# Kernel tuning notes

Hardware: AMD Instinct MI355X
Metric: run time of the kernel (lower is better)

Reference implementation:

```python
import jax, jax.numpy as jnp
import numpy as np

N = 50000    # num genes (nodes)
E = 500000   # edges per edge type
T = 2        # edge types
L = 2        # gnn layers
H = 4        # attention heads
D = 64       # per-head channels (hidden // heads)
HID = 256    # hidden channels
PRE_IN = 1024
OUT = 64
EPS = 1e-5
SLOPE = 0.2  # PyG GATv2 leaky_relu negative slope


def _layer_norm(x, g, b):
    mu = x.mean(-1, keepdims=True)
    v = x.var(-1, keepdims=True)
    return (x - mu) / jnp.sqrt(v + EPS) * g + b


def _seg_softmax(score, seg, n):
    m = jax.ops.segment_max(score, seg, num_segments=n)
    ex = jnp.exp(score - m[seg])
    den = jax.ops.segment_sum(ex, seg, num_segments=n)
    return ex / (den[seg] + 1e-16)


def _gatv2_projected(x, src, dst, Wl, Wr, att, bias, Wp, bp):
    # GATv2Conv (share_weights=False, concat heads) followed by Linear projection
    n = x.shape[0]
    xl = (x @ Wl).reshape(n, H, D)
    xr = (x @ Wr).reshape(n, H, D)
    hs = xl[src]                                   # [E,H,D] messages from source
    e = jax.nn.leaky_relu(hs + xr[dst], SLOPE)     # [E,H,D]
    score = jnp.einsum('ehd,hd->eh', e, att)       # [E,H]
    alpha = _seg_softmax(score, dst, n)            # softmax over in-edges of dst
    out = jax.ops.segment_sum(hs * alpha[:, :, None], dst, num_segments=n)
    out = out.reshape(n, H * D) + bias             # concat heads + conv bias
    return out @ Wp + bp                           # ProjectedGATConv linear


def setup_inputs() -> dict:
    key = jax.random.key(0)
    ks = jax.random.split(key, 20)
    s = 0.05
    return {
        'x': jax.random.normal(ks[0], (N, PRE_IN), dtype=jnp.float32),
        'edge_index_0': jax.random.randint(ks[1], (2, E), 0, N, dtype=jnp.int32),
        'edge_index_1': jax.random.randint(ks[2], (2, E), 0, N, dtype=jnp.int32),
        'pre_W0': jax.random.normal(ks[3], (PRE_IN, HID)) * s,
        'pre_b0': jnp.zeros((HID,)),
        'pre_g0': jnp.ones((HID,)),
        'pre_be0': jnp.zeros((HID,)),
        'pre_W1': jax.random.normal(ks[4], (HID, HID)) * s,
        'pre_b1': jnp.zeros((HID,)),
        'pre_g1': jnp.ones((HID,)),
        'pre_be1': jnp.zeros((HID,)),
        # HeteroGnn: L layers x T edge types of ProjectedGATConv(GATv2)
        'gat_Wl': jax.random.normal(ks[5], (L, T, HID, H * D)) * s,
        'gat_Wr': jax.random.normal(ks[6], (L, T, HID, H * D)) * s,
        'gat_att': jax.random.normal(ks[7], (L, T, H, D)) * 0.1,
        'gat_bias': jnp.zeros((L, T, H * D)),
        'proj_W': jax.random.normal(ks[8], (L, T, H * D, HID)) * s,
        'proj_b': jnp.zeros((L, T, HID)),
        # prediction head: Linear(HID,HID) + relu + Linear(HID,OUT)
        'head_W0': jax.random.normal(ks[9], (HID, HID)) * s,
        'head_b0': jnp.zeros((HID,)),
        'head_W1': jax.random.normal(ks[10], (HID, OUT)) * s,
        'head_b1': jnp.zeros((OUT,)),
    }


def reference(x, edge_index_0, edge_index_1, pre_W0, pre_b0, pre_g0, pre_be0,
              pre_W1, pre_b1, pre_g1, pre_be1, gat_Wl, gat_Wr, gat_att,
              gat_bias, proj_W, proj_b, head_W0, head_b0, head_W1, head_b1):
    loop = jnp.arange(N, dtype=edge_index_0.dtype)  # add_self_loops=True
    edges = [(jnp.concatenate([ei[0], loop]), jnp.concatenate([ei[1], loop]))
             for ei in (edge_index_0, edge_index_1)]
    # preprocessor MLP
    h = jax.nn.relu(_layer_norm(x @ pre_W0 + pre_b0, pre_g0, pre_be0))
    h = jax.nn.relu(_layer_norm(h @ pre_W1 + pre_b1, pre_g1, pre_be1))
    # hetero GAT stack, HeteroConv aggr='sum'
    for l in range(L):
        acc = jnp.zeros((N, HID), dtype=h.dtype)
        for t in range(T):
            src, dst = edges[t]
            acc = acc + _gatv2_projected(h, src, dst, gat_Wl[l, t], gat_Wr[l, t],
                                         gat_att[l, t], gat_bias[l, t],
                                         proj_W[l, t], proj_b[l, t])
        h = jax.nn.relu(acc)
    # prediction head
    h2 = jax.nn.relu(h @ head_W0 + head_b0)
    return h2 @ head_W1 + head_b1
```

## Files before the change

kernel.cpp:

```cpp
#include <hip/hip_runtime.h>
#include <hip/hip_bf16.h>
#include <math.h>

#define N_NODES 50000
#define MP      50048
#define E_EDGES 500000
#define EPRIME  (E_EDGES + N_NODES)
#define HID     256
#define PRE_IN  1024
#define OUT_DIM 64
#define NHEAD   4
#define DHEAD   64
#define LAYERS  2
#define NTYPES  2

#define SCAN_NBLK 49
#define NPAD      (SCAN_NBLK * 1024)

typedef __attribute__((ext_vector_type(8))) short short8v;
typedef __attribute__((ext_vector_type(4))) float f32x4;
typedef _Float16 h2v __attribute__((ext_vector_type(2)));
typedef _Float16 h8v __attribute__((ext_vector_type(8)));

__device__ __forceinline__ ushort f2bf(float f) {
  uint u = __float_as_uint(f);
  u += 0x7FFF + ((u >> 16) & 1);
  return (ushort)(u >> 16);
}
__device__ __forceinline__ float bf2f(ushort u) {
  return __uint_as_float(((uint)u) << 16);
}

template<bool AF32>
__global__ __launch_bounds__(256) void gemm_k(
    const void* __restrict__ Ap,
    const ushort* __restrict__ Bt,
    int K, int M, int N,
    float*  __restrict__ Cf,
    ushort* __restrict__ Cb,
    const float* __restrict__ bias,
    const float* __restrict__ bias2,
    int do_relu, int out_f16)
{
  __shared__ ushort As[128 * 32];
  __shared__ ushort Bs[64 * 32];
  const int tid = threadIdx.x;
  const int l   = tid & 63;
  const int w   = tid >> 6;
  const int wm  = w & 1;
  const int wn  = w >> 1;

  const int nwg  = gridDim.x * gridDim.y;
  const int orig = blockIdx.y * gridDim.x + blockIdx.x;
  const int qq   = nwg >> 3, rr = nwg & 7;
  const int xcd  = orig & 7;
  const int wgid = ((xcd < rr) ? xcd * (qq + 1) : rr * (qq + 1) + (xcd - rr) * qq)
                   + (orig >> 3);
  const int bm = (wgid / gridDim.x) * 128;
  const int bn = (wgid % gridDim.x) * 64;

  f32x4 acc[4][2];
#pragma unroll
  for (int m = 0; m < 4; m++)
#pragma unroll
    for (int n = 0; n < 2; n++) acc[m][n] = (f32x4){0.f, 0.f, 0.f, 0.f};

  const int srow  = l >> 2;
  const int sslot = l & 3;

  const int brow  = tid >> 2;
  const int bslot = tid & 3;
  const int bkc   = bslot ^ ((brow >> 1) & 3);

  float4 pf[2][2];
  if constexpr (AF32) {
#pragma unroll
    for (int i = 0; i < 2; i++) {
      const int row = w * 32 + i * 16 + srow;
      const int kc  = sslot ^ ((row >> 1) & 3);
      pf[i][0] = make_float4(0.f, 0.f, 0.f, 0.f);
      pf[i][1] = make_float4(0.f, 0.f, 0.f, 0.f);
      if (bm + row < M) {
        const float* ga = (const float*)Ap + (size_t)(bm + row) * K + kc * 8;
        pf[i][0] = *reinterpret_cast<const float4*>(ga);
        pf[i][1] = *reinterpret_cast<const float4*>(ga + 4);
      }
    }
  }

  for (int k0 = 0; k0 < K; k0 += 32) {
    {
      const ushort* gb = Bt + (size_t)(bn + brow) * K + k0 + bkc * 8;
      __builtin_amdgcn_global_load_lds(
          (const __attribute__((address_space(1))) uint*)gb,
          (__attribute__((address_space(3))) uint*)((char*)Bs + tid * 16), 16, 0, 0);
    }
    if constexpr (AF32) {
#pragma unroll
      for (int i = 0; i < 2; i++) {
        const int row = w * 32 + i * 16 + srow;
        const uint off = (uint)row * 64 + (uint)sslot * 16;
        short8v s;
        s[0] = (short)f2bf(pf[i][0].x); s[1] = (short)f2bf(pf[i][0].y);
        s[2] = (short)f2bf(pf[i][0].z); s[3] = (short)f2bf(pf[i][0].w);
        s[4] = (short)f2bf(pf[i][1].x); s[5] = (short)f2bf(pf[i][1].y);
        s[6] = (short)f2bf(pf[i][1].z); s[7] = (short)f2bf(pf[i][1].w);
        *reinterpret_cast<short8v*>((char*)As + off) = s;
      }
      if (k0 + 32 < K) {
#pragma unroll
        for (int i = 0; i < 2; i++) {
          const int row = w * 32 + i * 16 + srow;
          const int kc  = sslot ^ ((row >> 1) & 3);
          if (bm + row < M) {
            const float* ga = (const float*)Ap + (size_t)(bm + row) * K + (k0 + 32) + kc * 8;
            pf[i][0] = *reinterpret_cast<const float4*>(ga);
            pf[i][1] = *reinterpret_cast<const float4*>(ga + 4);
          }
        }
      }
    } else {
#pragma unroll
      for (int i = 0; i < 2; i++) {
        const int row = w * 32 + i * 16 + srow;
        const int kc  = sslot ^ ((row >> 1) & 3);
        const uint off = (uint)row * 64 + (uint)sslot * 16;
        const ushort* ga = (const ushort*)Ap + (size_t)(bm + row) * K + k0 + kc * 8;
        __builtin_amdgcn_global_load_lds(
            (const __attribute__((address_space(1))) uint*)ga,
            (__attribute__((address_space(3))) uint*)((char*)As + off), 16, 0, 0);
      }
    }
    __syncthreads();

    short8v a[4], b[2];
#pragma unroll
    for (int m = 0; m < 4; m++) {
      const int row = wm * 64 + m * 16 + (l & 15);
      const int kc  = (l >> 4) ^ ((row >> 1) & 3);
      a[m] = *(const short8v*)((const char*)As + row * 64 + kc * 16);
    }
#pragma unroll
    for (int n = 0; n < 2; n++) {
      const int row = wn * 32 + n * 16 + (l & 15);
      const int kc  = (l >> 4) ^ ((row >> 1) & 3);
      b[n] = *(const short8v*)((const char*)Bs + row * 64 + kc * 16);
    }
#pragma unroll
    for (int m = 0; m < 4; m++)
#pragma unroll
      for (int n = 0; n < 2; n++)
        acc[m][n] = __builtin_amdgcn_mfma_f32_16x16x32_bf16(a[m], b[n], acc[m][n], 0, 0, 0);
    __syncthreads();
  }

  const int crow0 = bm + wm * 64 + (l >> 4) * 4;
  const int ccol0 = bn + wn * 32 + (l & 15);
#pragma unroll
  for (int m = 0; m < 4; m++) {
#pragma unroll
    for (int j = 0; j < 4; j++) {
      const int grow = crow0 + m * 16 + j;
      if (grow < M) {
#pragma unroll
        for (int n = 0; n < 2; n++) {
          const int gcol = ccol0 + n * 16;
          if (gcol < N) {
            float v = acc[m][n][j];
            if (bias)  v += bias[gcol];
            if (bias2) v += bias2[gcol];
            if (do_relu) v = fmaxf(v, 0.f);
            if (Cf) Cf[(size_t)grow * N + gcol] = v;
            else if (out_f16) {
              _Float16 hv = (_Float16)v;
              Cb[(size_t)grow * N + gcol] = *(ushort*)&hv;
            } else {
              Cb[(size_t)grow * N + gcol] = f2bf(v);
            }
          }
        }
      }
    }
  }
}

__global__ void ln_relu(const float* __restrict__ in, ushort* __restrict__ out,
                        const float* __restrict__ g, const float* __restrict__ be, int n)
{
  int gid = blockIdx.x * blockDim.x + threadIdx.x;
  int row = gid >> 6;
  int lane = threadIdx.x & 63;
  if (row >= n) return;
  float4 v = *reinterpret_cast<const float4*>(in + (size_t)row * HID + lane * 4);
  float s = v.x + v.y + v.z + v.w;
  float ss = v.x * v.x + v.y * v.y + v.z * v.z + v.w * v.w;
#pragma unroll
  for (int o = 1; o < 64; o <<= 1) { s += __shfl_xor(s, o); ss += __shfl_xor(ss, o); }
  float mu = s * (1.f / 256.f);
  float var = ss * (1.f / 256.f) - mu * mu;
  float inv = rsqrtf(var + 1e-5f);
  float4 gg = *reinterpret_cast<const float4*>(g + lane * 4);
  float4 bb = *reinterpret_cast<const float4*>(be + lane * 4);
  ushort4 o4;
  o4.x = f2bf(fmaxf((v.x - mu) * inv * gg.x + bb.x, 0.f));
  o4.y = f2bf(fmaxf((v.y - mu) * inv * gg.y + bb.y, 0.f));
  o4.z = f2bf(fmaxf((v.z - mu) * inv * gg.z + bb.z, 0.f));
  o4.w = f2bf(fmaxf((v.w - mu) * inv * gg.w + bb.w, 0.f));
  *reinterpret_cast<ushort4*>(out + (size_t)row * HID + lane * 4) = o4;
}

__global__ void csr_count2(const int* __restrict__ ei0, const int* __restrict__ ei1,
                           int* __restrict__ cnt0, int* __restrict__ cnt1)
{
  int e = blockIdx.x * blockDim.x + threadIdx.x;
  if (e >= 2 * EPRIME) return;
  int type = e >= EPRIME;
  int i = type ? e - EPRIME : e;
  const int* ei = type ? ei1 : ei0;
  int* cnt = type ? cnt1 : cnt0;
  int d = (i < E_EDGES) ? ei[E_EDGES + i] : (i - E_EDGES);
  atomicAdd(&cnt[d], 1);
}

__global__ __launch_bounds__(256) void scan_p1(const int* __restrict__ cnt0,
                                               const int* __restrict__ cnt1,
                                               int* __restrict__ bsums)
{
  int type = blockIdx.x >= SCAN_NBLK;
  int blk = type ? blockIdx.x - SCAN_NBLK : blockIdx.x;
  const int* cnt = type ? cnt1 : cnt0;
  int4 v = reinterpret_cast<const int4*>(cnt)[blk * 256 + threadIdx.x];
  int s = v.x + v.y + v.z + v.w;
#pragma unroll
  for (int o = 1; o < 64; o <<= 1) s += __shfl_xor(s, o);
  __shared__ int wt[4];
  if ((threadIdx.x & 63) == 0) wt[threadIdx.x >> 6] = s;
  __syncthreads();
  if (threadIdx.x == 0) bsums[blockIdx.x] = wt[0] + wt[1] + wt[2] + wt[3];
}

__global__ void scan_p2(const int* __restrict__ bsums, int* __restrict__ boffs,
                        int* __restrict__ offs0, int* __restrict__ offs1)
{
  int t = threadIdx.x;
  if (t < 2) {
    int run = 0;
    for (int i = 0; i < SCAN_NBLK; i++) {
      boffs[t * SCAN_NBLK + i] = run;
      run += bsums[t * SCAN_NBLK + i];
    }
  }
  if (t == 2) offs0[N_NODES] = EPRIME;
  if (t == 3) offs1[N_NODES] = EPRIME;
}

__global__ __launch_bounds__(256) void scan_p3(
    const int* __restrict__ cnt0, const int* __restrict__ cnt1,
    const int* __restrict__ boffs,
    int* __restrict__ offs0, int* __restrict__ cur0,
    int* __restrict__ offs1, int* __restrict__ cur1)
{
  int type = blockIdx.x >= SCAN_NBLK;
  int blk = type ? blockIdx.x - SCAN_NBLK : blockIdx.x;
  const int* cnt = type ? cnt1 : cnt0;
  int* offs = type ? offs1 : offs0;
  int* cur  = type ? cur1 : cur0;
  const int tid = threadIdx.x, lane = tid & 63, wv = tid >> 6;
  int4 v = reinterpret_cast<const int4*>(cnt)[blk * 256 + tid];
  int e1 = v.x, e2 = e1 + v.y, e3 = e2 + v.z, T = e3 + v.w;
  int incl = T;
#pragma unroll
  for (int o = 1; o < 64; o <<= 1) {
    int nb = __shfl_up(incl, o);
    if (lane >= o) incl += nb;
  }
  __shared__ int wt[4];
  if (lane == 63) wt[wv] = incl;
  __syncthreads();
  int wexcl = 0;
  for (int i = 0; i < wv; i++) wexcl += wt[i];
  int base = boffs[blockIdx.x] + wexcl + (incl - T);
  int idx = blk * 1024 + tid * 4;
  int4 o4 = make_int4(base, base + e1, base + e2, base + e3);
  if (idx + 3 < N_NODES) {
    reinterpret_cast<int4*>(offs)[idx >> 2] = o4;
    reinterpret_cast<int4*>(cur)[idx >> 2] = o4;
  } else {
    if (idx + 0 < N_NODES) { offs[idx + 0] = o4.x; cur[idx + 0] = o4.x; }
    if (idx + 1 < N_NODES) { offs[idx + 1] = o4.y; cur[idx + 1] = o4.y; }
    if (idx + 2 < N_NODES) { offs[idx + 2] = o4.z; cur[idx + 2] = o4.z; }
    if (idx + 3 < N_NODES) { offs[idx + 3] = o4.w; cur[idx + 3] = o4.w; }
  }
}

__global__ void csr_scatter2(const int* __restrict__ ei0, const int* __restrict__ ei1,
                             int* __restrict__ cur0, int* __restrict__ cur1,
                             int* __restrict__ csr0, int* __restrict__ csr1)
{
  int e = blockIdx.x * blockDim.x + threadIdx.x;
  if (e >= 2 * EPRIME) return;
  int type = e >= EPRIME;
  int i = type ? e - EPRIME : e;
  const int* ei = type ? ei1 : ei0;
  int* cur = type ? cur1 : cur0;
  int* csr = type ? csr1 : csr0;
  int d = (i < E_EDGES) ? ei[E_EDGES + i] : (i - E_EDGES);
  int s = (i < E_EDGES) ? ei[i] : (i - E_EDGES);
  int pos = atomicAdd(&cur[d], 1);
  csr[pos] = s;
}

__global__ void csr_sort2(const int* __restrict__ offs0, int* __restrict__ csr0,
                          const int* __restrict__ offs1, int* __restrict__ csr1)
{
  int d = blockIdx.x * blockDim.x + threadIdx.x;
  if (d >= 2 * N_NODES) return;
  int type = d >= N_NODES;
  int i = type ? d - N_NODES : d;
  const int* offs = type ? offs1 : offs0;
  int* csr = type ? csr1 : csr0;
  int b = offs[i], e = offs[i + 1];
  for (int p = b + 1; p < e; p++) {
    int v = csr[p];
    int j = p - 1;
    while (j >= b && csr[j] > v) { csr[j + 1] = csr[j]; j--; }
    csr[j + 1] = v;
  }
}

#define WSEG0 262144
#define WSEG1 (WSEG0 + 65536)
#define WSEG2 (WSEG1 + 524288)
#define WSEG3 (WSEG2 + 262144)
#define WSEG4 (WSEG3 + 65536)
#define WSEG5 (WSEG4 + 32768)
__global__ void wtrans_all(const float* __restrict__ pre_W0, const float* __restrict__ pre_W1,
                           const float* __restrict__ Wl, const float* __restrict__ Wr,
                           const float* __restrict__ proj_W,
                           const float* __restrict__ head_W0, const float* __restrict__ head_W1,
                           ushort* __restrict__ W0t, ushort* __restrict__ W1t,
                           ushort* __restrict__ WcatT, ushort* __restrict__ projcatT,
                           ushort* __restrict__ hW0t, ushort* __restrict__ hW1t)
{
  int i = blockIdx.x * blockDim.x + threadIdx.x;
  if (i < WSEG0) {
    int nrow = i >> 10, k = i & 1023;
    W0t[i] = f2bf(pre_W0[(size_t)k * 256 + nrow]);
  } else if (i < WSEG1) {
    int j = i - WSEG0;
    int nrow = j >> 8, k = j & 255;
    W1t[j] = f2bf(pre_W1[(size_t)k * 256 + nrow]);
  } else if (i < WSEG2) {
    int j = i - WSEG1;
    int l = j >> 18;
    int rem = j & 262143;
    int c = rem >> 8, k = rem & 255;
    int t = c >> 9, half = (c >> 8) & 1, cc = c & 255;
    const float* W = half ? Wr : Wl;
    WcatT[j] = f2bf(W[(((size_t)l * NTYPES + t) * 256 + k) * 256 + cc]);
  } else if (i < WSEG3) {
    int j = i - WSEG2;
    int l = j >> 17;
    int rem = j & 131071;
    int n = rem >> 9, k = rem & 511;
    int t = k >> 8, kk = k & 255;
    projcatT[j] = f2bf(proj_W[(((size_t)l * NTYPES + t) * 256 + kk) * 256 + n]);
  } else if (i < WSEG4) {
    int j = i - WSEG3;
    int nrow = j >> 8, k = j & 255;
    hW0t[j] = f2bf(head_W0[(size_t)k * 256 + nrow]);
  } else if (i < WSEG5) {
    int j = i - WSEG4;
    int nrow = j >> 8, k = j & 255;
    hW1t[j] = (nrow < OUT_DIM) ? f2bf(head_W1[(size_t)k * OUT_DIM + nrow]) : (ushort)0;
  }
}

__device__ __forceinline__ float dpp8_sum(float p) {
  p += __int_as_float(__builtin_amdgcn_update_dpp(0, __float_as_int(p), 0xB1, 0xF, 0xF, true));
  p += __int_as_float(__builtin_amdgcn_update_dpp(0, __float_as_int(p), 0x4E, 0xF, 0xF, true));
  p += __int_as_float(__builtin_amdgcn_update_dpp(0, __float_as_int(p), 0x141, 0xF, 0xF, true));
  return p;
}

__device__ __forceinline__ h8v leaky8(h8v x) {
  const _Float16 c = (_Float16)0.2f;
  h8v y = x * c;
#if __has_builtin(__builtin_elementwise_max)
  return __builtin_elementwise_max(x, y);
#else
  h8v r;
#pragma unroll
  for (int i = 0; i < 8; i++) r[i] = x[i] > y[i] ? x[i] : y[i];
  return r;
#endif
}

__device__ __forceinline__ float dot8(h8v e, const h2v* a) {
  h2v e0 = {e[0], e[1]}, e1 = {e[2], e[3]}, e2 = {e[4], e[5]}, e3 = {e[6], e[7]};
#if __has_builtin(__builtin_amdgcn_fdot2)
  float s = __builtin_amdgcn_fdot2(e0, a[0], 0.f, false);
  s = __builtin_amdgcn_fdot2(e1, a[1], s, false);
  s = __builtin_amdgcn_fdot2(e2, a[2], s, false);
  s = __builtin_amdgcn_fdot2(e3, a[3], s, false);
  return s;
#else
  float s = 0.f;
#pragma unroll
  for (int i = 0; i < 8; i++) s += (float)e[i] * (float)a[i >> 1][i & 1];
  return s;
#endif
}

__global__ __launch_bounds__(256) void gat_edge3(
    const _Float16* __restrict__ xlr,
    const int* __restrict__ offs0, const int* __restrict__ csr0,
    const int* __restrict__ offs1, const int* __restrict__ csr1,
    const float* __restrict__ att,
    const float* __restrict__ bias,
    ushort* __restrict__ out, int nblk_per_type)
{
  const int type = blockIdx.x >= nblk_per_type;
  const int bid = type ? blockIdx.x - nblk_per_type : blockIdx.x;
  const int wid = (bid * 256 + threadIdx.x) >> 6;
  if (wid >= N_NODES) return;
  const int lane = threadIdx.x & 63;
  const int half = lane >> 5, li = lane & 31;
  const int* offs = type ? offs1 : offs0;
  const int* csr  = type ? csr1 : csr0;
  const int xl_col = type ? 512 : 0;

  const float* ap = att + type * 256 + li * 8;
  h2v a[4];
#pragma unroll
  for (int i = 0; i < 4; i++) {
    a[i][0] = (_Float16)ap[2 * i];
    a[i][1] = (_Float16)ap[2 * i + 1];
  }
  const h8v xr = *reinterpret_cast<const h8v*>(xlr + (size_t)wid * 1024 + xl_col + 256 + li * 8);

  const int beg = offs[wid], end = offs[wid + 1];
  const float L2E = 1.44269504f;
  float m = -1e30f, den = 0.f;
  float acc[8];
#pragma unroll
  for (int i = 0; i < 8; i++) acc[i] = 0.f;

  const int ng = (end - beg + 3) >> 2;
  for (int g = 0; g < ng; g++) {
    const int j0 = beg + 4 * g + half;
    const int j1 = j0 + 2;
    const bool v0 = j0 < end, v1 = j1 < end;
    const int s0 = csr[v0 ? j0 : beg];
    const int s1 = csr[v1 ? j1 : beg];
    const h8v hs0 = *reinterpret_cast<const h8v*>(xlr + (size_t)s0 * 1024 + xl_col + li * 8);
    const h8v hs1 = *reinterpret_cast<const h8v*>(xlr + (size_t)s1 * 1024 + xl_col + li * 8);
    float p0 = dpp8_sum(dot8(leaky8(hs0 + xr), a));
    float p1 = dpp8_sum(dot8(leaky8(hs1 + xr), a));
    if (!v0) p0 = -INFINITY;
    if (!v1) p1 = -INFINITY;
    const float pm = fmaxf(p0, p1);
    if (__any(pm > m + 4.f)) {
      const float nm = fmaxf(m, pm);
      const float so = exp2f((m - nm) * L2E);
      den *= so;
#pragma unroll
      for (int i = 0; i < 8; i++) acc[i] *= so;
      m = nm;
    }
    const float w0 = exp2f((p0 - m) * L2E);
    const float w1 = exp2f((p1 - m) * L2E);
    den += w0 + w1;
#pragma unroll
    for (int i = 0; i < 8; i++) {
      acc[i] = fmaf((float)hs0[i], w0, acc[i]);
      acc[i] = fmaf((float)hs1[i], w1, acc[i]);
    }
  }

  const float mo  = __shfl_xor(m, 32);
  const float dno = __shfl_xor(den, 32);
  const float ms = fmaxf(m, mo);
  const float fa = exp2f((m - ms) * L2E);
  const float fb = exp2f((mo - ms) * L2E);
  const float r = 1.f / (den * fa + dno * fb + 1e-16f);
  float of[8];
#pragma unroll
  for (int i = 0; i < 8; i++)
    of[i] = (acc[i] * fa + __shfl_xor(acc[i], 32) * fb) * r;

  if (half == 0) {
    const float* bp = bias + type * 256 + li * 8;
    uint4 o;
    uint pk[4];
#pragma unroll
    for (int i = 0; i < 4; i++) {
      const uint lo = f2bf(of[2 * i] + bp[2 * i]);
      const uint hi = f2bf(of[2 * i + 1] + bp[2 * i + 1]);
      pk[i] = lo | (hi << 16);
    }
    o.x = pk[0]; o.y = pk[1]; o.z = pk[2]; o.w = pk[3];
    *reinterpret_cast<uint4*>(out + (size_t)wid * 512 + type * 256 + li * 8) = o;
  }
}

extern "C" void kernel_launch(void* const* d_in, const int* in_sizes, int n_in,
                              void* d_out, int out_size, void* d_ws, size_t ws_size,
                              hipStream_t stream)
{
  const float* x        = (const float*)d_in[0];
  const int*   ei0      = (const int*)d_in[1];
  const int*   ei1      = (const int*)d_in[2];
  const float* pre_W0   = (const float*)d_in[3];
  const float* pre_b0   = (const float*)d_in[4];
  const float* pre_g0   = (const float*)d_in[5];
  const float* pre_be0  = (const float*)d_in[6];
  const float* pre_W1   = (const float*)d_in[7];
  const float* pre_b1   = (const float*)d_in[8];
  const float* pre_g1   = (const float*)d_in[9];
  const float* pre_be1  = (const float*)d_in[10];
  const float* gat_Wl   = (const float*)d_in[11];
  const float* gat_Wr   = (const float*)d_in[12];
  const float* gat_att  = (const float*)d_in[13];
  const float* gat_bias = (const float*)d_in[14];
  const float* proj_W   = (const float*)d_in[15];
  const float* proj_b   = (const float*)d_in[16];
  const float* head_W0  = (const float*)d_in[17];
  const float* head_b0  = (const float*)d_in[18];
  const float* head_W1  = (const float*)d_in[19];
  const float* head_b1  = (const float*)d_in[20];
  float* outp = (float*)d_out;

  char* ws = (char*)d_ws;
  ushort* xlr_b = (ushort*)ws; ws += (size_t)MP * 1024 * 2;
  ushort* hb    = (ushort*)ws; ws += (size_t)MP * 256 * 2;
  ushort* outt  = (ushort*)ws; ws += (size_t)MP * 512 * 2;
  float*  tmp   = (float*)outt;
  ushort* hbuf  = (ushort*)outt;
  ushort* W0t      = (ushort*)ws; ws += (size_t)256 * 1024 * 2;
  ushort* W1t      = (ushort*)ws; ws += (size_t)256 * 256 * 2;
  ushort* WcatT    = (ushort*)ws; ws += (size_t)LAYERS * 1024 * 256 * 2;
  ushort* projcatT = (ushort*)ws; ws += (size_t)LAYERS * 256 * 512 * 2;
  ushort* hW0t     = (ushort*)ws; ws += (size_t)256 * 256 * 2;
  ushort* hW1t     = (ushort*)ws; ws += (size_t)128 * 256 * 2;
  int* cnt0  = (int*)ws; ws += (size_t)NPAD * 4;
  int* cnt1  = (int*)ws; ws += (size_t)NPAD * 4;
  int* offs0 = (int*)ws; ws += (size_t)(N_NODES + 4) * 4;
  int* offs1 = (int*)ws; ws += (size_t)(N_NODES + 4) * 4;
  int* cur0  = (int*)ws; ws += (size_t)N_NODES * 4;
  int* cur1  = (int*)ws; ws += (size_t)N_NODES * 4;
  int* bsums = (int*)ws; ws += (size_t)128 * 4;
  int* boffs = (int*)ws; ws += (size_t)128 * 4;
  int* csr0  = (int*)ws; ws += (size_t)EPRIME * 4;
  int* csr1  = (int*)ws; ws += (size_t)EPRIME * 4;

  hipMemsetAsync(cnt0, 0, (size_t)2 * NPAD * 4, stream);
  const int gE2 = (2 * EPRIME + 255) / 256;
  csr_count2<<<gE2, 256, 0, stream>>>(ei0, ei1, cnt0, cnt1);
  scan_p1<<<2 * SCAN_NBLK, 256, 0, stream>>>(cnt0, cnt1, bsums);
  scan_p2<<<1, 64, 0, stream>>>(bsums, boffs, offs0, offs1);
  scan_p3<<<2 * SCAN_NBLK, 256, 0, stream>>>(cnt0, cnt1, boffs, offs0, cur0, offs1, cur1);
  csr_scatter2<<<gE2, 256, 0, stream>>>(ei0, ei1, cur0, cur1, csr0, csr1);
  csr_sort2<<<(2 * N_NODES + 255) / 256, 256, 0, stream>>>(offs0, csr0, offs1, csr1);

  wtrans_all<<<WSEG5 / 256, 256, 0, stream>>>(pre_W0, pre_W1, gat_Wl, gat_Wr, proj_W,
                                              head_W0, head_W1,
                                              W0t, W1t, WcatT, projcatT, hW0t, hW1t);

  const dim3 blk(256);
  const int gy = MP / 128;
  const int gln = (N_NODES * 64 + 255) / 256;

  gemm_k<true><<<dim3(4, gy), blk, 0, stream>>>(x, W0t, 1024, N_NODES, 256,
                                                tmp, nullptr, pre_b0, nullptr, 0, 0);
  ln_relu<<<gln, 256, 0, stream>>>(tmp, hb, pre_g0, pre_be0, N_NODES);
  gemm_k<false><<<dim3(4, gy), blk, 0, stream>>>(hb, W1t, 256, N_NODES, 256,
                                                 tmp, nullptr, pre_b1, nullptr, 0, 0);
  ln_relu<<<gln, 256, 0, stream>>>(tmp, hb, pre_g1, pre_be1, N_NODES);

  for (int l = 0; l < LAYERS; l++) {
    gemm_k<false><<<dim3(16, gy), blk, 0, stream>>>(hb, WcatT + (size_t)l * 1024 * 256,
                                                    256, N_NODES, 1024,
                                                    nullptr, xlr_b, nullptr, nullptr, 0, 1);
    gat_edge3<<<2 * gln, 256, 0, stream>>>(
        (const _Float16*)xlr_b, offs0, csr0, offs1, csr1,
        gat_att  + (size_t)l * NTYPES * NHEAD * DHEAD,
        gat_bias + (size_t)l * NTYPES * HID,
        outt, gln);
    gemm_k<false><<<dim3(4, gy), blk, 0, stream>>>(
        outt, projcatT + (size_t)l * 256 * 512, 512, N_NODES, 256,
        nullptr, hb,
        proj_b + (size_t)(l * NTYPES + 0) * HID,
        proj_b + (size_t)(l * NTYPES + 1) * HID, 1, 0);
  }

  gemm_k<false><<<dim3(4, gy), blk, 0, stream>>>(hb, hW0t, 256, N_NODES, 256,
                                                 nullptr, hbuf, head_b0, nullptr, 1, 0);
  gemm_k<false><<<dim3(1, gy), blk, 0, stream>>>(hbuf, hW1t, 256, N_NODES, OUT_DIM,
                                                 outp, nullptr, head_b1, nullptr, 0, 0);
}
```

Before: 778.6 us.

## Triple-buffer GEMM LDS tiles and prefetch two k-steps ahead

The bf16 MFMA GEMM moves from a single LDS buffer with two barriers per k-step to a three-stage ring buffer. Global-to-LDS loads for tile t+2 are issued before the MFMAs on tile t. Each iteration ends with one barrier guarded by explicit vmcnt/lgkmcnt waits and scheduling barriers. The aim is to hide global-load latency behind compute and cut synchronization, at the cost of three times the LDS footprint, which may reduce occupancy. Correctness now rests on hand-written wait counts.

```diff
diff --git a/kernel.cpp b/kernel.cpp
--- a/kernel.cpp
+++ b/kernel.cpp
@@ -31,6 +31,12 @@
   return __uint_as_float(((uint)u) << 16);
 }
 
+#define WAITV3 asm volatile("s_waitcnt vmcnt(3)" ::: "memory")
+#define WAITV0 asm volatile("s_waitcnt vmcnt(0)" ::: "memory")
+#define WAITLG asm volatile("s_waitcnt lgkmcnt(0)" ::: "memory")
+#define SCHEDB __builtin_amdgcn_sched_barrier(0)
+#define BARRIER __builtin_amdgcn_s_barrier()
+
 template<bool AF32>
 __global__ __launch_bounds__(256) void gemm_k(
     const void* __restrict__ Ap,
@@ -42,8 +48,8 @@
     const float* __restrict__ bias2,
     int do_relu, int out_f16)
 {
-  __shared__ ushort As[128 * 32];
-  __shared__ ushort Bs[64 * 32];
+  __shared__ ushort As[3][128 * 32];
+  __shared__ ushort Bs[3][64 * 32];
   const int tid = threadIdx.x;
   const int l   = tid & 63;
   const int w   = tid >> 6;
@@ -67,7 +73,16 @@
 
   const int srow  = l >> 2;
   const int sslot = l & 3;
-
+  const int nt    = K >> 5;
+
+  int  arow[2], akc[2];
+  uint aoff[2];
+#pragma unroll
+  for (int i = 0; i < 2; i++) {
+    arow[i] = w * 32 + i * 16 + srow;
+    akc[i]  = sslot ^ ((arow[i] >> 1) & 3);
+    aoff[i] = (uint)arow[i] * 64 + (uint)sslot * 16;
+  }
   const int brow  = tid >> 2;
   const int bslot = tid & 3;
   const int bkc   = bslot ^ ((brow >> 1) & 3);
@@ -76,82 +91,105 @@
   if constexpr (AF32) {
 #pragma unroll
     for (int i = 0; i < 2; i++) {
-      const int row = w * 32 + i * 16 + srow;
-      const int kc  = sslot ^ ((row >> 1) & 3);
       pf[i][0] = make_float4(0.f, 0.f, 0.f, 0.f);
       pf[i][1] = make_float4(0.f, 0.f, 0.f, 0.f);
-      if (bm + row < M) {
-        const float* ga = (const float*)Ap + (size_t)(bm + row) * K + kc * 8;
-        pf[i][0] = *reinterpret_cast<const float4*>(ga);
-        pf[i][1] = *reinterpret_cast<const float4*>(ga + 4);
-      }
-    }
-  }
-
-  for (int k0 = 0; k0 < K; k0 += 32) {
-    {
-      const ushort* gb = Bt + (size_t)(bn + brow) * K + k0 + bkc * 8;
-      __builtin_amdgcn_global_load_lds(
-          (const __attribute__((address_space(1))) uint*)gb,
-          (__attribute__((address_space(3))) uint*)((char*)Bs + tid * 16), 16, 0, 0);
-    }
+    }
+  }
+
+#define STAGE_B(t, buf)                                                        \
+  {                                                                            \
+    const ushort* gb = Bt + (size_t)(bn + brow) * K + ((t) << 5) + bkc * 8;    \
+    __builtin_amdgcn_global_load_lds(                                          \
+        (const __attribute__((address_space(1))) uint*)gb,                     \
+        (__attribute__((address_space(3))) uint*)((char*)Bs[buf] + tid * 16),  \
+        16, 0, 0);                                                             \
+  }
+#define STAGE_A16(t, buf)                                                      \
+  _Pragma("unroll")                                                            \
+  for (int i = 0; i < 2; i++) {                                                \
+    const ushort* ga = (const ushort*)Ap + (size_t)(bm + arow[i]) * K +        \
+                       ((t) << 5) + akc[i] * 8;                                \
+    __builtin_amdgcn_global_load_lds(                                          \
+        (const __attribute__((address_space(1))) uint*)ga,                     \
+        (__attribute__((address_space(3))) uint*)((char*)As[buf] + aoff[i]),   \
+        16, 0, 0);                                                             \
+  }
+#define LOAD_A32(t)                                                            \
+  _Pragma("unroll")                                                            \
+  for (int i = 0; i < 2; i++) {                                                \
+    if (bm + arow[i] < M) {                                                    \
+      const float* ga = (const float*)Ap + (size_t)(bm + arow[i]) * K +        \
+                        ((t) << 5) + akc[i] * 8;                               \
+      pf[i][0] = *reinterpret_cast<const float4*>(ga);                         \
+      pf[i][1] = *reinterpret_cast<const float4*>(ga + 4);                     \
+    }                                                                          \
+  }
+#define WRITE_A32(buf)                                                         \
+  _Pragma("unroll")                                                            \
+  for (int i = 0; i < 2; i++) {                                                \
+    short8v s;                                                                 \
+    s[0] = (short)f2bf(pf[i][0].x); s[1] = (short)f2bf(pf[i][0].y);            \
+    s[2] = (short)f2bf(pf[i][0].z); s[3] = (short)f2bf(pf[i][0].w);            \
+    s[4] = (short)f2bf(pf[i][1].x); s[5] = (short)f2bf(pf[i][1].y);            \
+    s[6] = (short)f2bf(pf[i][1].z); s[7] = (short)f2bf(pf[i][1].w);            \
+    *reinterpret_cast<short8v*>((char*)As[buf] + aoff[i]) = s;                 \
+  }
+
+  if constexpr (AF32) {
+    STAGE_B(0, 0);
+    LOAD_A32(0);
+    WRITE_A32(0);
+    STAGE_B(1, 1);
+    LOAD_A32(1);
+    WAITLG; SCHEDB; BARRIER; SCHEDB;
+  } else {
+    STAGE_B(0, 0); STAGE_A16(0, 0);
+    STAGE_B(1, 1); STAGE_A16(1, 1);
+    WAITV3;
+    SCHEDB; BARRIER; SCHEDB;
+  }
+
+  int rd = 0;
+  for (int t = 0; t < nt; t++) {
+    int wr = rd + 1; if (wr == 3) wr = 0;
+    int st = wr + 1; if (st == 3) st = 0;
+
     if constexpr (AF32) {
-#pragma unroll
-      for (int i = 0; i < 2; i++) {
-        const int row = w * 32 + i * 16 + srow;
-        const uint off = (uint)row * 64 + (uint)sslot * 16;
-        short8v s;
-        s[0] = (short)f2bf(pf[i][0].x); s[1] = (short)f2bf(pf[i][0].y);
-        s[2] = (short)f2bf(pf[i][0].z); s[3] = (short)f2bf(pf[i][0].w);
-        s[4] = (short)f2bf(pf[i][1].x); s[5] = (short)f2bf(pf[i][1].y);
-        s[6] = (short)f2bf(pf[i][1].z); s[7] = (short)f2bf(pf[i][1].w);
-        *reinterpret_cast<short8v*>((char*)As + off) = s;
-      }
-      if (k0 + 32 < K) {
-#pragma unroll
-        for (int i = 0; i < 2; i++) {
-          const int row = w * 32 + i * 16 + srow;
-          const int kc  = sslot ^ ((row >> 1) & 3);
-          if (bm + row < M) {
-            const float* ga = (const float*)Ap + (size_t)(bm + row) * K + (k0 + 32) + kc * 8;
-            pf[i][0] = *reinterpret_cast<const float4*>(ga);
-            pf[i][1] = *reinterpret_cast<const float4*>(ga + 4);
-          }
-        }
-      }
+      if (t + 1 < nt) WRITE_A32(wr);
+      if (t + 2 < nt) { STAGE_B(t + 2, st); LOAD_A32(t + 2); }
     } else {
-#pragma unroll
-      for (int i = 0; i < 2; i++) {
-        const int row = w * 32 + i * 16 + srow;
-        const int kc  = sslot ^ ((row >> 1) & 3);
-        const uint off = (uint)row * 64 + (uint)sslot * 16;
-        const ushort* ga = (const ushort*)Ap + (size_t)(bm + row) * K + k0 + kc * 8;
-        __builtin_amdgcn_global_load_lds(
-            (const __attribute__((address_space(1))) uint*)ga,
-            (__attribute__((address_space(3))) uint*)((char*)As + off), 16, 0, 0);
-      }
-    }
-    __syncthreads();
+      if (t + 2 < nt) { STAGE_B(t + 2, st); STAGE_A16(t + 2, st); }
+    }
 
     short8v a[4], b[2];
 #pragma unroll
     for (int m = 0; m < 4; m++) {
       const int row = wm * 64 + m * 16 + (l & 15);
       const int kc  = (l >> 4) ^ ((row >> 1) & 3);
-      a[m] = *(const short8v*)((const char*)As + row * 64 + kc * 16);
+      a[m] = *(const short8v*)((const char*)As[rd] + row * 64 + kc * 16);
     }
 #pragma unroll
     for (int n = 0; n < 2; n++) {
       const int row = wn * 32 + n * 16 + (l & 15);
       const int kc  = (l >> 4) ^ ((row >> 1) & 3);
-      b[n] = *(const short8v*)((const char*)Bs + row * 64 + kc * 16);
+      b[n] = *(const short8v*)((const char*)Bs[rd] + row * 64 + kc * 16);
     }
 #pragma unroll
     for (int m = 0; m < 4; m++)
 #pragma unroll
       for (int n = 0; n < 2; n++)
         acc[m][n] = __builtin_amdgcn_mfma_f32_16x16x32_bf16(a[m], b[n], acc[m][n], 0, 0, 0);
-    __syncthreads();
+
+    if (t + 1 < nt) {
+      if constexpr (AF32) {
+        WAITLG;
+      } else {
+        if (t + 2 < nt) { WAITV3; }
+        else            { WAITV0; }
+      }
+      SCHEDB; BARRIER; SCHEDB;
+    }
+    rd = wr;
   }
 
   const int crow0 = bm + wm * 64 + (l >> 4) * 4;
```

After: 816.4 us. 4.9% more time.
